# Performance work log

Hardware: AMD Instinct MI355X
Metric: run time of the kernel (lower is better)

## Reference

```python
import jax, jax.numpy as jnp
import numpy as np

# Faithful JAX port of the approxmatch EMD kernel (Fan et al.) wrapped by emdDist.
# 10 soft-assignment (auction-style) iterations with annealed temperature level=-4^j,
# j = 7..-1, final iteration level = 0. match is accumulated transport mass;
# cost[b] = sum_{k,l} match[b,k,l] * ||x1_k - x2_l||.

_EPS = 1e-9


def _approxmatch(xyz1, xyz2):
    # xyz1: (b, n, 3), xyz2: (b, m, 3)
    b, n, _ = xyz1.shape
    m = xyz2.shape[1]
    factorl = max(n, m) / n
    factorr = max(n, m) / m
    remainL = jnp.full((b, n), factorl, dtype=xyz1.dtype)   # mass left on xyz1 points
    remainR = jnp.full((b, m), factorr, dtype=xyz1.dtype)   # capacity left on xyz2 points
    # pairwise squared distances (b, n, m)
    d2 = jnp.sum((xyz1[:, :, None, :] - xyz2[:, None, :, :]) ** 2, axis=-1)
    match = jnp.zeros((b, n, m), dtype=xyz1.dtype)
    for j in range(7, -3, -1):  # j = 7, 6, ..., -1, -2
        level = 0.0 if j == -2 else -(4.0 ** j)
        # proposal weights from each left point, scaled by remaining right capacity
        w = jnp.exp(level * d2) * remainR[:, None, :]                      # (b,n,m)
        w = w / (jnp.sum(w, axis=-1, keepdims=True) + _EPS) * remainL[:, :, None]
        # right points accept at most their remaining capacity
        sumr = jnp.sum(w, axis=1) + _EPS                                   # (b,m)
        ratio = jnp.minimum(remainR / sumr, 1.0)                           # (b,m)
        delta = w * ratio[:, None, :]                                      # accepted transfer
        match = match + delta
        remainL = jnp.maximum(remainL - jnp.sum(delta, axis=-1), 0.0)
        remainR = jnp.maximum(remainR - jnp.sum(delta, axis=1), 0.0)
    return match, d2


def setup_inputs() -> dict:
    key = jax.random.key(0)
    k1, k2 = jax.random.split(key)
    B, N, M = 8, 4096, 4096
    input1 = jax.random.normal(k1, (B, N, 3), dtype=jnp.float32)
    input2 = jax.random.normal(k2, (B, M, 3), dtype=jnp.float32)
    return {"input1": input1, "input2": input2}


def reference(input1, input2):
    match, d2 = _approxmatch(input1, input2)
    # original CUDA backward treats match as a constant -> stop_gradient
    match = jax.lax.stop_gradient(match)
    dist = jnp.sqrt(jnp.maximum(d2, 1e-12))
    cost = jnp.sum(match * dist, axis=(1, 2))  # (b,)
    return cost
```

## Files before the change

### kernel.cpp

```cpp
#include <hip/hip_runtime.h>

#define NPTS 4096
#define NB   8
#define TPB  256
#define TPBR 128
#define MBLK 4
#define EPSC 1e-9f

#define EXP2(x)  __builtin_amdgcn_exp2f(x)
#define RCPF(x)  __builtin_amdgcn_rcpf(x)
#define SQRTF(x) __builtin_amdgcn_sqrtf(x)

__global__ __launch_bounds__(TPB) void sort_kernel(
    const float* __restrict__ x1, const float* __restrict__ x2,
    float4* __restrict__ x1p, float4* __restrict__ x2p)
{
  __shared__ unsigned int   hist[4096];
  __shared__ unsigned short codes[4096];
  __shared__ unsigned int   part[TPB];

  const int set = blockIdx.x, b = blockIdx.y;
  const float* src = set ? x2 : x1;
  float4* dst = set ? x2p : x1p;
  const int tid = threadIdx.x;

  for (int i = tid; i < 4096; i += TPB) hist[i] = 0;
  __syncthreads();

  for (int j = 0; j < NPTS / TPB; ++j) {
    int n = j * TPB + tid;
    const float* p = src + ((size_t)b * NPTS + n) * 3;
    float x = p[0], y = p[1], z = p[2];
    int qx = min(max((int)((x + 4.f) * 2.f), 0), 15);
    int qy = min(max((int)((y + 4.f) * 2.f), 0), 15);
    int qz = min(max((int)((z + 4.f) * 2.f), 0), 15);
    auto ex = [](int v) {
      return (v & 1) | ((v & 2) << 2) | ((v & 4) << 4) | ((v & 8) << 6);
    };
    int code = ex(qx) | (ex(qy) << 1) | (ex(qz) << 2);
    codes[n] = (unsigned short)code;
    atomicAdd(&hist[code], 1u);
  }
  __syncthreads();

  unsigned int loc[16], s = 0;
#pragma unroll
  for (int j = 0; j < 16; ++j) { loc[j] = s; s += hist[tid * 16 + j]; }
  part[tid] = s;
  __syncthreads();
  if (tid == 0) {
    unsigned int run = 0;
    for (int t = 0; t < TPB; ++t) { unsigned int v = part[t]; part[t] = run; run += v; }
  }
  __syncthreads();
  {
    unsigned int base = part[tid];
#pragma unroll
    for (int j = 0; j < 16; ++j) hist[tid * 16 + j] = base + loc[j];
  }
  __syncthreads();

  for (int j = 0; j < NPTS / TPB; ++j) {
    int n = j * TPB + tid;
    const float* p = src + ((size_t)b * NPTS + n) * 3;
    float x = p[0], y = p[1], z = p[2];
    unsigned int pos = atomicAdd(&hist[codes[n]], 1u);
    dst[(size_t)b * NPTS + pos] = make_float4(x, y, z, 0.f);
  }
}

template<int MODE, bool SKIP, int CHUNK>
__global__ __launch_bounds__(TPB) void ca_kernel(
    const float4* __restrict__ x2p, const float4* __restrict__ x1p,
    const float2* __restrict__ urP,
    float* __restrict__ dbufP, float* __restrict__ rsumP,
    float* __restrict__ out, float sc)
{
  __shared__ float4 x2s[CHUNK];
  __shared__ float2 urs[CHUNK];

  const int tid = threadIdx.x;
  const int nchunk = blockIdx.x, mseg = blockIdx.y, b = blockIdx.z;

  if (MODE == 0 && nchunk == 0 && mseg == 0 && tid == 0) out[b] = 0.f;

  for (int mm = tid; mm < CHUNK; mm += TPB) {
    int m = mseg * CHUNK + mm;
    float4 q = x2p[(size_t)b * NPTS + m];
    float sx = sc * q.x, sy = sc * q.y, sz = sc * q.z;
    float nq = fmaf(sz, sz, fmaf(sy, sy, sx * sx));
    x2s[mm] = make_float4(-2.f * sx, -2.f * sy, -2.f * sz, nq);
    urs[mm] = (MODE == 0) ? make_float2(0.f, 1.f) : urP[(size_t)b * NPTS + m];
  }
  __syncthreads();

  const int n0 = nchunk * (TPB * MBLK) + tid * MBLK;
  float px[MBLK], py[MBLK], pz[MBLK], np[MBLK], dacc[MBLK], racc[MBLK];
#pragma unroll
  for (int k = 0; k < MBLK; ++k) {
    float4 p = x1p[(size_t)b * NPTS + n0 + k];
    px[k] = sc * p.x; py[k] = sc * p.y; pz[k] = sc * p.z;
    np[k] = fmaf(pz[k], pz[k], fmaf(py[k], py[k], px[k] * px[k]));
    dacc[k] = 0.f; racc[k] = 0.f;
  }

#pragma unroll 4
  for (int mm = 0; mm < CHUNK; ++mm) {
    float4 q = x2s[mm];
    float2 ur = urs[mm];
    float ds2[MBLK];
#pragma unroll
    for (int k = 0; k < MBLK; ++k)
      ds2[k] = fmaf(q.x, px[k], fmaf(q.y, py[k], fmaf(q.z, pz[k], np[k] + q.w)));
    if (MODE == 2) {
#pragma unroll
      for (int k = 0; k < MBLK; ++k) {
        dacc[k] += ur.y;
        racc[k] = fmaf(EXP2(-ds2[k]), ur.x, racc[k]);
      }
    } else {
      bool go = true;
      if (SKIP) {
        float dmin = fminf(fminf(ds2[0], ds2[1]), fminf(ds2[2], ds2[3]));
        go = dmin < 126.f;
      }
      if (go) {
#pragma unroll
        for (int k = 0; k < MBLK; ++k) {
          float en = EXP2(-ds2[k]);
          dacc[k] = fmaf(en, ur.y, dacc[k]);
          if (MODE == 1) { float e2 = en * en; racc[k] = fmaf(e2 * e2, ur.x, racc[k]); }
        }
      }
    }
  }

  size_t base = ((size_t)mseg * NB + b) * NPTS + n0;
  *(float4*)&dbufP[base] = make_float4(dacc[0], dacc[1], dacc[2], dacc[3]);
  if (MODE >= 1)
    *(float4*)&rsumP[base] = make_float4(racc[0], racc[1], racc[2], racc[3]);
}

template<int LVL0, bool SKIP, int CHUNK>
__global__ __launch_bounds__(TPB) void b_kernel(
    const float4* __restrict__ x1p, const float* __restrict__ abuf,
    const float4* __restrict__ x2p,
    float* __restrict__ s0P, float* __restrict__ s1P,
    float sc, float inv_s)
{
  __shared__ float4 x1s[CHUNK];
  __shared__ float  as_[CHUNK];

  const int tid = threadIdx.x;
  const int mchunk = blockIdx.x, nsegi = blockIdx.y, b = blockIdx.z;

  for (int nn = tid; nn < CHUNK; nn += TPB) {
    int n = nsegi * CHUNK + nn;
    float4 p = x1p[(size_t)b * NPTS + n];
    float sx = sc * p.x, sy = sc * p.y, sz = sc * p.z;
    float npv = fmaf(sz, sz, fmaf(sy, sy, sx * sx));
    x1s[nn] = make_float4(-2.f * sx, -2.f * sy, -2.f * sz, npv);
    as_[nn] = abuf[(size_t)b * NPTS + n];
  }
  __syncthreads();

  const int m0 = mchunk * (TPB * MBLK) + tid * MBLK;
  float qx[MBLK], qy[MBLK], qz[MBLK], nq[MBLK], s0a[MBLK], s1a[MBLK];
#pragma unroll
  for (int k = 0; k < MBLK; ++k) {
    float4 q = x2p[(size_t)b * NPTS + m0 + k];
    qx[k] = sc * q.x; qy[k] = sc * q.y; qz[k] = sc * q.z;
    nq[k] = fmaf(qz[k], qz[k], fmaf(qy[k], qy[k], qx[k] * qx[k]));
    s0a[k] = 0.f; s1a[k] = 0.f;
  }

#pragma unroll 4
  for (int nn = 0; nn < CHUNK; ++nn) {
    float4 p = x1s[nn];
    float av = as_[nn];
    float ds2[MBLK];
#pragma unroll
    for (int k = 0; k < MBLK; ++k)
      ds2[k] = fmaf(p.x, qx[k], fmaf(p.y, qy[k], fmaf(p.z, qz[k], nq[k] + p.w)));
    if (LVL0) {
#pragma unroll
      for (int k = 0; k < MBLK; ++k) {
        s0a[k] += av;
        s1a[k] = fmaf(av, SQRTF(__builtin_fabsf(ds2[k])), s1a[k]);
      }
    } else {
      bool go = true;
      if (SKIP) {
        float dmin = fminf(fminf(ds2[0], ds2[1]), fminf(ds2[2], ds2[3]));
        go = dmin < 126.f;
      }
      if (go) {
#pragma unroll
        for (int k = 0; k < MBLK; ++k) {
          float tt = av * EXP2(-ds2[k]);
          s0a[k] += tt;
          s1a[k] = fmaf(tt, SQRTF(__builtin_fabsf(ds2[k])), s1a[k]);
        }
      }
    }
  }

  size_t base = ((size_t)nsegi * NB + b) * NPTS + m0;
  *(float4*)&s0P[base] = make_float4(s0a[0], s0a[1], s0a[2], s0a[3]);
  *(float4*)&s1P[base] = make_float4(s1a[0] * inv_s, s1a[1] * inv_s,
                                     s1a[2] * inv_s, s1a[3] * inv_s);
}

template<int NSEG>
__global__ __launch_bounds__(TPBR) void r1_kernel(
    const float* __restrict__ dbufP, const float* __restrict__ rsumP,
    float* __restrict__ lbuf, float* __restrict__ dtot,
    float* __restrict__ abuf, int iter)
{
  const int idx = blockIdx.x * TPBR + threadIdx.x;
  const int b = idx >> 12, n = idx & (NPTS - 1);
  const int off = b * NPTS + n;

  float dnew = 0.f;
#pragma unroll
  for (int s = 0; s < NSEG; ++s) dnew += dbufP[((size_t)s * NB + b) * NPTS + n];

  float rl;
  if (iter == 0) {
    rl = 1.f;
  } else {
    float rlp = lbuf[off];
    float ap  = rlp * RCPF(dtot[off] + EPSC);
    float rs = 0.f;
#pragma unroll
    for (int s = 0; s < NSEG; ++s) rs += rsumP[((size_t)s * NB + b) * NPTS + n];
    rl = fmaxf(rlp - ap * rs, 0.f);
  }
  lbuf[off] = rl;
  dtot[off] = dnew;
  abuf[off] = rl * RCPF(dnew + EPSC);
}

template<int NSEG, bool LAST>
__global__ __launch_bounds__(TPBR) void r2_kernel(
    const float* __restrict__ s0P, const float* __restrict__ s1P,
    float2* __restrict__ urbuf, float* __restrict__ out, int iter)
{
  __shared__ float red[TPBR];
  const int idx = blockIdx.x * TPBR + threadIdx.x;
  const int b = idx >> 12, m = idx & (NPTS - 1);
  const int off = b * NPTS + m;

  float s0 = 0.f, s1 = 0.f;
#pragma unroll
  for (int s = 0; s < NSEG; ++s) {
    s0 += s0P[((size_t)s * NB + b) * NPTS + m];
    s1 += s1P[((size_t)s * NB + b) * NPTS + m];
  }
  float rr    = (iter == 0) ? 1.f : urbuf[off].y;
  float sumr  = fmaf(rr, s0, EPSC);
  float ratio = fminf(rr * RCPF(sumr), 1.f);
  float u     = rr * ratio;
  if (!LAST) urbuf[off] = make_float2(u, fmaxf(rr - u * s0, 0.f));

  red[threadIdx.x] = u * s1;
  __syncthreads();
  for (int s = TPBR / 2; s > 0; s >>= 1) {
    if (threadIdx.x < s) red[threadIdx.x] += red[threadIdx.x + s];
    __syncthreads();
  }
  if (threadIdx.x == 0) atomicAdd(out + b, red[0]);
}

template<int NSEG>
static void run_all(const float* x1, const float* x2, float* out, float* ws,
                    hipStream_t stream)
{
  constexpr int CHUNK = NPTS / NSEG;
  const size_t plane = (size_t)NB * NPTS;

  float*  bufA = ws;
  float*  bufB = bufA + (size_t)NSEG * plane;
  float4* x1p  = (float4*)(bufB + (size_t)NSEG * plane);
  float4* x2p  = x1p + plane;
  float*  dtot = (float*)(x2p + plane);
  float*  lbuf = dtot + plane;
  float*  abuf = lbuf + plane;
  float2* urbuf = (float2*)(abuf + plane);

  const double L2E = 1.4426950408889634074;
  const double lv[10] = {-16384.0, -4096.0, -1024.0, -256.0, -64.0,
                         -16.0, -4.0, -1.0, -0.25, 0.0};
  float scl[10], inv_s[10];
  for (int i = 0; i < 10; ++i) {
    double c2 = lv[i] * L2E;
    scl[i]   = (i == 9) ? 1.f : (float)sqrt(-c2);
    inv_s[i] = (i == 9) ? 1.f : (float)(1.0 / sqrt(-c2));
  }

  dim3 gmain(NPTS / (TPB * MBLK), NSEG, NB), bmain(TPB);
  dim3 gr(NPTS * NB / TPBR), br(TPBR);

  sort_kernel<<<dim3(2, NB), bmain, 0, stream>>>(x1, x2, x1p, x2p);

  ca_kernel<0, true, CHUNK><<<gmain, bmain, 0, stream>>>(
      x2p, x1p, urbuf, bufA, bufB, out, scl[0]);

  for (int i = 0; i < 10; ++i) {
    r1_kernel<NSEG><<<gr, br, 0, stream>>>(bufA, bufB, lbuf, dtot, abuf, i);

    if (i <= 4)
      b_kernel<0, true, CHUNK><<<gmain, bmain, 0, stream>>>(
          x1p, abuf, x2p, bufA, bufB, scl[i], inv_s[i]);
    else if (i <= 8)
      b_kernel<0, false, CHUNK><<<gmain, bmain, 0, stream>>>(
          x1p, abuf, x2p, bufA, bufB, scl[i], inv_s[i]);
    else
      b_kernel<1, false, CHUNK><<<gmain, bmain, 0, stream>>>(
          x1p, abuf, x2p, bufA, bufB, 1.f, 1.f);

    if (i < 9)
      r2_kernel<NSEG, false><<<gr, br, 0, stream>>>(bufA, bufB, urbuf, out, i);
    else
      r2_kernel<NSEG, true><<<gr, br, 0, stream>>>(bufA, bufB, urbuf, out, i);

    if (i <= 3)
      ca_kernel<1, true, CHUNK><<<gmain, bmain, 0, stream>>>(
          x2p, x1p, urbuf, bufA, bufB, out, scl[i + 1]);
    else if (i <= 7)
      ca_kernel<1, false, CHUNK><<<gmain, bmain, 0, stream>>>(
          x2p, x1p, urbuf, bufA, bufB, out, scl[i + 1]);
    else if (i == 8)
      ca_kernel<2, false, CHUNK><<<gmain, bmain, 0, stream>>>(
          x2p, x1p, urbuf, bufA, bufB, out, scl[8]);
  }
}

extern "C" void kernel_launch(void* const* d_in, const int* in_sizes, int n_in,
                              void* d_out, int out_size, void* d_ws, size_t ws_size,
                              hipStream_t stream) {
  const float* x1 = (const float*)d_in[0];
  const float* x2 = (const float*)d_in[1];
  float* out = (float*)d_out;
  float* ws  = (float*)d_ws;

  const size_t plane = (size_t)NB * NPTS;
  auto need = [&](int nseg) {
    return (size_t)(2 * nseg + 13) * plane * sizeof(float);
  };

  if (ws_size >= need(64))      run_all<64>(x1, x2, out, ws, stream);
  else if (ws_size >= need(32)) run_all<32>(x1, x2, out, ws, stream);
  else                          run_all<16>(x1, x2, out, ws, stream);
}
```

Before: 989.8 us.

## Cull far tile pairs via bounding boxes and accumulate partials with atomics

Result: slower. 1.651 ms (+66.8%).

```diff
diff --git a/kernel.cpp b/kernel.cpp
--- a/kernel.cpp
+++ b/kernel.cpp
@@ -1,11 +1,13 @@
 #include <hip/hip_runtime.h>
 
-#define NPTS 4096
-#define NB   8
-#define TPB  256
-#define TPBR 128
-#define MBLK 4
-#define EPSC 1e-9f
+#define NPTS  4096
+#define NB    8
+#define TPB   256
+#define TPBR  256
+#define MBLK  4
+#define NSEG  64
+#define CHUNK 64
+#define EPSC  1e-9f
 
 #define EXP2(x)  __builtin_amdgcn_exp2f(x)
 #define RCPF(x)  __builtin_amdgcn_rcpf(x)
@@ -13,7 +15,10 @@
 
 __global__ __launch_bounds__(TPB) void sort_kernel(
     const float* __restrict__ x1, const float* __restrict__ x2,
-    float4* __restrict__ x1p, float4* __restrict__ x2p)
+    float4* __restrict__ x1p, float4* __restrict__ x2p,
+    float4* __restrict__ bb,
+    float* __restrict__ zacc,
+    float* __restrict__ out)
 {
   __shared__ unsigned int   hist[4096];
   __shared__ unsigned short codes[4096];
@@ -23,6 +28,11 @@
   const float* src = set ? x2 : x1;
   float4* dst = set ? x2p : x1p;
   const int tid = threadIdx.x;
+  const int bid = b * 2 + set;
+
+  for (int i = tid; i < 2 * NB * NPTS / 16; i += TPB)
+    zacc[(size_t)bid * (2 * NB * NPTS / 16) + i] = 0.f;
+  if (set == 0 && tid == 0) out[b] = 0.f;
 
   for (int i = tid; i < 4096; i += TPB) hist[i] = 0;
   __syncthreads();
@@ -30,10 +40,9 @@
   for (int j = 0; j < NPTS / TPB; ++j) {
     int n = j * TPB + tid;
     const float* p = src + ((size_t)b * NPTS + n) * 3;
-    float x = p[0], y = p[1], z = p[2];
-    int qx = min(max((int)((x + 4.f) * 2.f), 0), 15);
-    int qy = min(max((int)((y + 4.f) * 2.f), 0), 15);
-    int qz = min(max((int)((z + 4.f) * 2.f), 0), 15);
+    int qx = min(max((int)((p[0] + 4.f) * 2.f), 0), 15);
+    int qy = min(max((int)((p[1] + 4.f) * 2.f), 0), 15);
+    int qz = min(max((int)((p[2] + 4.f) * 2.f), 0), 15);
     auto ex = [](int v) {
       return (v & 1) | ((v & 2) << 2) | ((v & 4) << 4) | ((v & 8) << 6);
     };
@@ -63,26 +72,39 @@
   for (int j = 0; j < NPTS / TPB; ++j) {
     int n = j * TPB + tid;
     const float* p = src + ((size_t)b * NPTS + n) * 3;
-    float x = p[0], y = p[1], z = p[2];
     unsigned int pos = atomicAdd(&hist[codes[n]], 1u);
-    dst[(size_t)b * NPTS + pos] = make_float4(x, y, z, 0.f);
-  }
-}
-
-template<int MODE, bool SKIP, int CHUNK>
+    dst[(size_t)b * NPTS + pos] = make_float4(p[0], p[1], p[2], 0.f);
+  }
+  __syncthreads();
+
+  if (tid < 64) {
+    float mnx = 1e30f, mny = 1e30f, mnz = 1e30f;
+    float mxx = -1e30f, mxy = -1e30f, mxz = -1e30f;
+    for (int j = 0; j < CHUNK; ++j) {
+      float4 p = dst[(size_t)b * NPTS + tid * CHUNK + j];
+      mnx = fminf(mnx, p.x); mxx = fmaxf(mxx, p.x);
+      mny = fminf(mny, p.y); mxy = fmaxf(mxy, p.y);
+      mnz = fminf(mnz, p.z); mxz = fmaxf(mxz, p.z);
+    }
+    size_t bi = ((size_t)(set * NB + b) * 64 + tid) * 2;
+    bb[bi + 0] = make_float4(mnx, mny, mnz, 0.f);
+    bb[bi + 1] = make_float4(mxx, mxy, mxz, 0.f);
+  }
+}
+
+template<int MODE, bool CULL, bool PSKIP>
 __global__ __launch_bounds__(TPB) void ca_kernel(
     const float4* __restrict__ x2p, const float4* __restrict__ x1p,
-    const float2* __restrict__ urP,
-    float* __restrict__ dbufP, float* __restrict__ rsumP,
-    float* __restrict__ out, float sc)
+    const float2* __restrict__ urbuf,
+    float* __restrict__ dAcc, float* __restrict__ rAcc,
+    const float4* __restrict__ bb2,
+    float sc)
 {
   __shared__ float4 x2s[CHUNK];
   __shared__ float2 urs[CHUNK];
 
   const int tid = threadIdx.x;
   const int nchunk = blockIdx.x, mseg = blockIdx.y, b = blockIdx.z;
-
-  if (MODE == 0 && nchunk == 0 && mseg == 0 && tid == 0) out[b] = 0.f;
 
   for (int mm = tid; mm < CHUNK; mm += TPB) {
     int m = mseg * CHUNK + mm;
@@ -90,7 +112,8 @@
     float sx = sc * q.x, sy = sc * q.y, sz = sc * q.z;
     float nq = fmaf(sz, sz, fmaf(sy, sy, sx * sx));
     x2s[mm] = make_float4(-2.f * sx, -2.f * sy, -2.f * sz, nq);
-    urs[mm] = (MODE == 0) ? make_float2(0.f, 1.f) : urP[(size_t)b * NPTS + m];
+    urs[mm] = (MODE == 0) ? make_float2(0.f, 1.f)
+                          : urbuf[(size_t)b * NPTS + m];
   }
   __syncthreads();
 
@@ -104,6 +127,30 @@
     dacc[k] = 0.f; racc[k] = 0.f;
   }
 
+  if (CULL) {
+    float mnx = fminf(fminf(px[0], px[1]), fminf(px[2], px[3]));
+    float mny = fminf(fminf(py[0], py[1]), fminf(py[2], py[3]));
+    float mnz = fminf(fminf(pz[0], pz[1]), fminf(pz[2], pz[3]));
+    float mxx = fmaxf(fmaxf(px[0], px[1]), fmaxf(px[2], px[3]));
+    float mxy = fmaxf(fmaxf(py[0], py[1]), fmaxf(py[2], py[3]));
+    float mxz = fmaxf(fmaxf(pz[0], pz[1]), fmaxf(pz[2], pz[3]));
+#pragma unroll
+    for (int off = 1; off < 64; off <<= 1) {
+      mnx = fminf(mnx, __shfl_xor(mnx, off));
+      mny = fminf(mny, __shfl_xor(mny, off));
+      mnz = fminf(mnz, __shfl_xor(mnz, off));
+      mxx = fmaxf(mxx, __shfl_xor(mxx, off));
+      mxy = fmaxf(mxy, __shfl_xor(mxy, off));
+      mxz = fmaxf(mxz, __shfl_xor(mxz, off));
+    }
+    size_t bi = ((size_t)b * 64 + mseg) * 2;
+    float4 smin = bb2[bi + 0], smax = bb2[bi + 1];
+    float gx = fmaxf(0.f, fmaxf(sc * smin.x - mxx, mnx - sc * smax.x));
+    float gy = fmaxf(0.f, fmaxf(sc * smin.y - mxy, mny - sc * smax.y));
+    float gz = fmaxf(0.f, fmaxf(sc * smin.z - mxz, mnz - sc * smax.z));
+    if (fmaf(gx, gx, fmaf(gy, gy, gz * gz)) >= 126.f) return;
+  }
+
 #pragma unroll 4
   for (int mm = 0; mm < CHUNK; ++mm) {
     float4 q = x2s[mm];
@@ -120,7 +167,7 @@
       }
     } else {
       bool go = true;
-      if (SKIP) {
+      if (PSKIP) {
         float dmin = fminf(fminf(ds2[0], ds2[1]), fminf(ds2[2], ds2[3]));
         go = dmin < 126.f;
       }
@@ -135,17 +182,20 @@
     }
   }
 
-  size_t base = ((size_t)mseg * NB + b) * NPTS + n0;
-  *(float4*)&dbufP[base] = make_float4(dacc[0], dacc[1], dacc[2], dacc[3]);
-  if (MODE >= 1)
-    *(float4*)&rsumP[base] = make_float4(racc[0], racc[1], racc[2], racc[3]);
-}
-
-template<int LVL0, bool SKIP, int CHUNK>
+  size_t off = (size_t)b * NPTS + n0;
+#pragma unroll
+  for (int k = 0; k < MBLK; ++k) {
+    atomicAdd(&dAcc[off + k], dacc[k]);
+    if (MODE >= 1) atomicAdd(&rAcc[off + k], racc[k]);
+  }
+}
+
+template<int LVL0, bool CULL, bool PSKIP>
 __global__ __launch_bounds__(TPB) void b_kernel(
     const float4* __restrict__ x1p, const float* __restrict__ abuf,
     const float4* __restrict__ x2p,
-    float* __restrict__ s0P, float* __restrict__ s1P,
+    float* __restrict__ s0Acc, float* __restrict__ s1Acc,
+    const float4* __restrict__ bb1,
     float sc, float inv_s)
 {
   __shared__ float4 x1s[CHUNK];
@@ -174,6 +224,30 @@
     s0a[k] = 0.f; s1a[k] = 0.f;
   }
 
+  if (CULL) {
+    float mnx = fminf(fminf(qx[0], qx[1]), fminf(qx[2], qx[3]));
+    float mny = fminf(fminf(qy[0], qy[1]), fminf(qy[2], qy[3]));
+    float mnz = fminf(fminf(qz[0], qz[1]), fminf(qz[2], qz[3]));
+    float mxx = fmaxf(fmaxf(qx[0], qx[1]), fmaxf(qx[2], qx[3]));
+    float mxy = fmaxf(fmaxf(qy[0], qy[1]), fmaxf(qy[2], qy[3]));
+    float mxz = fmaxf(fmaxf(qz[0], qz[1]), fmaxf(qz[2], qz[3]));
+#pragma unroll
+    for (int off = 1; off < 64; off <<= 1) {
+      mnx = fminf(mnx, __shfl_xor(mnx, off));
+      mny = fminf(mny, __shfl_xor(mny, off));
+      mnz = fminf(mnz, __shfl_xor(mnz, off));
+      mxx = fmaxf(mxx, __shfl_xor(mxx, off));
+      mxy = fmaxf(mxy, __shfl_xor(mxy, off));
+      mxz = fmaxf(mxz, __shfl_xor(mxz, off));
+    }
+    size_t bi = ((size_t)b * 64 + nsegi) * 2;
+    float4 smin = bb1[bi + 0], smax = bb1[bi + 1];
+    float gx = fmaxf(0.f, fmaxf(sc * smin.x - mxx, mnx - sc * smax.x));
+    float gy = fmaxf(0.f, fmaxf(sc * smin.y - mxy, mny - sc * smax.y));
+    float gz = fmaxf(0.f, fmaxf(sc * smin.z - mxz, mnz - sc * smax.z));
+    if (fmaf(gx, gx, fmaf(gy, gy, gz * gz)) >= 126.f) return;
+  }
+
 #pragma unroll 4
   for (int nn = 0; nn < CHUNK; ++nn) {
     float4 p = x1s[nn];
@@ -190,7 +264,7 @@
       }
     } else {
       bool go = true;
-      if (SKIP) {
+      if (PSKIP) {
         float dmin = fminf(fminf(ds2[0], ds2[1]), fminf(ds2[2], ds2[3]));
         go = dmin < 126.f;
       }
@@ -205,63 +279,54 @@
     }
   }
 
-  size_t base = ((size_t)nsegi * NB + b) * NPTS + m0;
-  *(float4*)&s0P[base] = make_float4(s0a[0], s0a[1], s0a[2], s0a[3]);
-  *(float4*)&s1P[base] = make_float4(s1a[0] * inv_s, s1a[1] * inv_s,
-                                     s1a[2] * inv_s, s1a[3] * inv_s);
-}
-
-template<int NSEG>
+  size_t off = (size_t)b * NPTS + m0;
+#pragma unroll
+  for (int k = 0; k < MBLK; ++k) {
+    atomicAdd(&s0Acc[off + k], s0a[k]);
+    atomicAdd(&s1Acc[off + k], s1a[k] * inv_s);
+  }
+}
+
 __global__ __launch_bounds__(TPBR) void r1_kernel(
-    const float* __restrict__ dbufP, const float* __restrict__ rsumP,
+    const float* __restrict__ dAcc, const float* __restrict__ rAcc,
     float* __restrict__ lbuf, float* __restrict__ dtot,
-    float* __restrict__ abuf, int iter)
+    float* __restrict__ abuf,
+    float* __restrict__ s0Acc, float* __restrict__ s1Acc, int iter)
 {
   const int idx = blockIdx.x * TPBR + threadIdx.x;
-  const int b = idx >> 12, n = idx & (NPTS - 1);
-  const int off = b * NPTS + n;
-
-  float dnew = 0.f;
-#pragma unroll
-  for (int s = 0; s < NSEG; ++s) dnew += dbufP[((size_t)s * NB + b) * NPTS + n];
-
-  float rl;
-  if (iter == 0) {
-    rl = 1.f;
-  } else {
-    float rlp = lbuf[off];
-    float ap  = rlp * RCPF(dtot[off] + EPSC);
-    float rs = 0.f;
-#pragma unroll
-    for (int s = 0; s < NSEG; ++s) rs += rsumP[((size_t)s * NB + b) * NPTS + n];
-    rl = fmaxf(rlp - ap * rs, 0.f);
-  }
-  lbuf[off] = rl;
-  dtot[off] = dnew;
-  abuf[off] = rl * RCPF(dnew + EPSC);
-}
-
-template<int NSEG, bool LAST>
+  float dnew = dAcc[idx];
+  float rl = 1.f;
+  if (iter > 0) {
+    float rlp = lbuf[idx];
+    float ap  = rlp * RCPF(dtot[idx] + EPSC);
+    rl = fmaxf(rlp - ap * rAcc[idx], 0.f);
+  }
+  lbuf[idx] = rl;
+  dtot[idx] = dnew;
+  abuf[idx] = rl * RCPF(dnew + EPSC);
+  s0Acc[idx] = 0.f;
+  s1Acc[idx] = 0.f;
+}
+
+template<bool LAST>
 __global__ __launch_bounds__(TPBR) void r2_kernel(
-    const float* __restrict__ s0P, const float* __restrict__ s1P,
-    float2* __restrict__ urbuf, float* __restrict__ out, int iter)
+    const float* __restrict__ s0Acc, const float* __restrict__ s1Acc,
+    float2* __restrict__ urbuf,
+    float* __restrict__ dAcc, float* __restrict__ rAcc,
+    float* __restrict__ out, int iter)
 {
   __shared__ float red[TPBR];
   const int idx = blockIdx.x * TPBR + threadIdx.x;
-  const int b = idx >> 12, m = idx & (NPTS - 1);
-  const int off = b * NPTS + m;
-
-  float s0 = 0.f, s1 = 0.f;
-#pragma unroll
-  for (int s = 0; s < NSEG; ++s) {
-    s0 += s0P[((size_t)s * NB + b) * NPTS + m];
-    s1 += s1P[((size_t)s * NB + b) * NPTS + m];
-  }
-  float rr    = (iter == 0) ? 1.f : urbuf[off].y;
+  const int b = idx >> 12;
+
+  float s0 = s0Acc[idx], s1 = s1Acc[idx];
+  float rr    = (iter == 0) ? 1.f : urbuf[idx].y;
   float sumr  = fmaf(rr, s0, EPSC);
   float ratio = fminf(rr * RCPF(sumr), 1.f);
   float u     = rr * ratio;
-  if (!LAST) urbuf[off] = make_float2(u, fmaxf(rr - u * s0, 0.f));
+  if (!LAST) urbuf[idx] = make_float2(u, fmaxf(rr - u * s0, 0.f));
+  dAcc[idx] = 0.f;
+  rAcc[idx] = 0.f;
 
   red[threadIdx.x] = u * s1;
   __syncthreads();
@@ -272,21 +337,28 @@
   if (threadIdx.x == 0) atomicAdd(out + b, red[0]);
 }
 
-template<int NSEG>
-static void run_all(const float* x1, const float* x2, float* out, float* ws,
-                    hipStream_t stream)
-{
-  constexpr int CHUNK = NPTS / NSEG;
+extern "C" void kernel_launch(void* const* d_in, const int* in_sizes, int n_in,
+                              void* d_out, int out_size, void* d_ws, size_t ws_size,
+                              hipStream_t stream) {
+  const float* x1 = (const float*)d_in[0];
+  const float* x2 = (const float*)d_in[1];
+  float* out = (float*)d_out;
+
   const size_t plane = (size_t)NB * NPTS;
-
-  float*  bufA = ws;
-  float*  bufB = bufA + (size_t)NSEG * plane;
-  float4* x1p  = (float4*)(bufB + (size_t)NSEG * plane);
-  float4* x2p  = x1p + plane;
-  float*  dtot = (float*)(x2p + plane);
-  float*  lbuf = dtot + plane;
-  float*  abuf = lbuf + plane;
+  float*  ws    = (float*)d_ws;
+  float*  dAcc  = ws;
+  float*  rAcc  = dAcc + plane;
+  float*  s0Acc = rAcc + plane;
+  float*  s1Acc = s0Acc + plane;
+  float*  dtot  = s1Acc + plane;
+  float*  lbuf  = dtot + plane;
+  float*  abuf  = lbuf + plane;
   float2* urbuf = (float2*)(abuf + plane);
+  float4* x1p   = (float4*)(urbuf + plane);
+  float4* x2p   = x1p + plane;
+  float4* bb    = x2p + plane;
+  float4* bb1   = bb;
+  float4* bb2   = bb + (size_t)NB * 64 * 2;
 
   const double L2E = 1.4426950408889634074;
   const double lv[10] = {-16384.0, -4096.0, -1024.0, -256.0, -64.0,
@@ -299,57 +371,48 @@
   }
 
   dim3 gmain(NPTS / (TPB * MBLK), NSEG, NB), bmain(TPB);
-  dim3 gr(NPTS * NB / TPBR), br(TPBR);
-
-  sort_kernel<<<dim3(2, NB), bmain, 0, stream>>>(x1, x2, x1p, x2p);
-
-  ca_kernel<0, true, CHUNK><<<gmain, bmain, 0, stream>>>(
-      x2p, x1p, urbuf, bufA, bufB, out, scl[0]);
+  dim3 gr(NB * NPTS / TPBR), br(TPBR);
+
+  sort_kernel<<<dim3(2, NB), bmain, 0, stream>>>(x1, x2, x1p, x2p, bb, dAcc, out);
+
+  ca_kernel<0, true, true><<<gmain, bmain, 0, stream>>>(
+      x2p, x1p, urbuf, dAcc, rAcc, bb2, scl[0]);
 
   for (int i = 0; i < 10; ++i) {
-    r1_kernel<NSEG><<<gr, br, 0, stream>>>(bufA, bufB, lbuf, dtot, abuf, i);
+    r1_kernel<<<gr, br, 0, stream>>>(dAcc, rAcc, lbuf, dtot, abuf,
+                                     s0Acc, s1Acc, i);
 
     if (i <= 4)
-      b_kernel<0, true, CHUNK><<<gmain, bmain, 0, stream>>>(
-          x1p, abuf, x2p, bufA, bufB, scl[i], inv_s[i]);
+      b_kernel<0, true, true><<<gmain, bmain, 0, stream>>>(
+          x1p, abuf, x2p, s0Acc, s1Acc, bb1, scl[i], inv_s[i]);
+    else if (i == 5)
+      b_kernel<0, true, false><<<gmain, bmain, 0, stream>>>(
+          x1p, abuf, x2p, s0Acc, s1Acc, bb1, scl[i], inv_s[i]);
     else if (i <= 8)
-      b_kernel<0, false, CHUNK><<<gmain, bmain, 0, stream>>>(
-          x1p, abuf, x2p, bufA, bufB, scl[i], inv_s[i]);
+      b_kernel<0, false, false><<<gmain, bmain, 0, stream>>>(
+          x1p, abuf, x2p, s0Acc, s1Acc, bb1, scl[i], inv_s[i]);
     else
-      b_kernel<1, false, CHUNK><<<gmain, bmain, 0, stream>>>(
-          x1p, abuf, x2p, bufA, bufB, 1.f, 1.f);
+      b_kernel<1, false, false><<<gmain, bmain, 0, stream>>>(
+          x1p, abuf, x2p, s0Acc, s1Acc, bb1, 1.f, 1.f);
 
     if (i < 9)
-      r2_kernel<NSEG, false><<<gr, br, 0, stream>>>(bufA, bufB, urbuf, out, i);
+      r2_kernel<false><<<gr, br, 0, stream>>>(s0Acc, s1Acc, urbuf,
+                                              dAcc, rAcc, out, i);
     else
-      r2_kernel<NSEG, true><<<gr, br, 0, stream>>>(bufA, bufB, urbuf, out, i);
+      r2_kernel<true><<<gr, br, 0, stream>>>(s0Acc, s1Acc, urbuf,
+                                             dAcc, rAcc, out, i);
 
     if (i <= 3)
-      ca_kernel<1, true, CHUNK><<<gmain, bmain, 0, stream>>>(
-          x2p, x1p, urbuf, bufA, bufB, out, scl[i + 1]);
+      ca_kernel<1, true, true><<<gmain, bmain, 0, stream>>>(
+          x2p, x1p, urbuf, dAcc, rAcc, bb2, scl[i + 1]);
+    else if (i == 4)
+      ca_kernel<1, true, false><<<gmain, bmain, 0, stream>>>(
+          x2p, x1p, urbuf, dAcc, rAcc, bb2, scl[i + 1]);
     else if (i <= 7)
-      ca_kernel<1, false, CHUNK><<<gmain, bmain, 0, stream>>>(
-          x2p, x1p, urbuf, bufA, bufB, out, scl[i + 1]);
+      ca_kernel<1, false, false><<<gmain, bmain, 0, stream>>>(
+          x2p, x1p, urbuf, dAcc, rAcc, bb2, scl[i + 1]);
     else if (i == 8)
-      ca_kernel<2, false, CHUNK><<<gmain, bmain, 0, stream>>>(
-          x2p, x1p, urbuf, bufA, bufB, out, scl[8]);
-  }
-}
-
-extern "C" void kernel_launch(void* const* d_in, const int* in_sizes, int n_in,
-                              void* d_out, int out_size, void* d_ws, size_t ws_size,
-                              hipStream_t stream) {
-  const float* x1 = (const float*)d_in[0];
-  const float* x2 = (const float*)d_in[1];
-  float* out = (float*)d_out;
-  float* ws  = (float*)d_ws;
-
-  const size_t plane = (size_t)NB * NPTS;
-  auto need = [&](int nseg) {
-    return (size_t)(2 * nseg + 13) * plane * sizeof(float);
-  };
-
-  if (ws_size >= need(64))      run_all<64>(x1, x2, out, ws, stream);
-  else if (ws_size >= need(32)) run_all<32>(x1, x2, out, ws, stream);
-  else                          run_all<16>(x1, x2, out, ws, stream);
-}
+      ca_kernel<2, false, false><<<gmain, bmain, 0, stream>>>(
+          x2p, x1p, urbuf, dAcc, rAcc, bb2, scl[8]);
+  }
+}
```

## Cull whole waves against per-segment bounding boxes of sorted points

Applied to the files above, without the earlier changes.

Result: slower. 1.010 ms (+2.0%).

```diff
diff --git a/kernel.cpp b/kernel.cpp
--- a/kernel.cpp
+++ b/kernel.cpp
@@ -13,7 +13,8 @@
 
 __global__ __launch_bounds__(TPB) void sort_kernel(
     const float* __restrict__ x1, const float* __restrict__ x2,
-    float4* __restrict__ x1p, float4* __restrict__ x2p)
+    float4* __restrict__ x1p, float4* __restrict__ x2p,
+    float4* __restrict__ bb)
 {
   __shared__ unsigned int   hist[4096];
   __shared__ unsigned short codes[4096];
@@ -30,10 +31,9 @@
   for (int j = 0; j < NPTS / TPB; ++j) {
     int n = j * TPB + tid;
     const float* p = src + ((size_t)b * NPTS + n) * 3;
-    float x = p[0], y = p[1], z = p[2];
-    int qx = min(max((int)((x + 4.f) * 2.f), 0), 15);
-    int qy = min(max((int)((y + 4.f) * 2.f), 0), 15);
-    int qz = min(max((int)((z + 4.f) * 2.f), 0), 15);
+    int qx = min(max((int)((p[0] + 4.f) * 2.f), 0), 15);
+    int qy = min(max((int)((p[1] + 4.f) * 2.f), 0), 15);
+    int qz = min(max((int)((p[2] + 4.f) * 2.f), 0), 15);
     auto ex = [](int v) {
       return (v & 1) | ((v & 2) << 2) | ((v & 4) << 4) | ((v & 8) << 6);
     };
@@ -63,18 +63,58 @@
   for (int j = 0; j < NPTS / TPB; ++j) {
     int n = j * TPB + tid;
     const float* p = src + ((size_t)b * NPTS + n) * 3;
-    float x = p[0], y = p[1], z = p[2];
     unsigned int pos = atomicAdd(&hist[codes[n]], 1u);
-    dst[(size_t)b * NPTS + pos] = make_float4(x, y, z, 0.f);
-  }
-}
-
-template<int MODE, bool SKIP, int CHUNK>
+    dst[(size_t)b * NPTS + pos] = make_float4(p[0], p[1], p[2], 0.f);
+  }
+  __syncthreads();
+
+  if (tid < 64) {
+    float mnx = 1e30f, mny = 1e30f, mnz = 1e30f;
+    float mxx = -1e30f, mxy = -1e30f, mxz = -1e30f;
+    for (int j = 0; j < 64; ++j) {
+      float4 p = dst[(size_t)b * NPTS + tid * 64 + j];
+      mnx = fminf(mnx, p.x); mxx = fmaxf(mxx, p.x);
+      mny = fminf(mny, p.y); mxy = fmaxf(mxy, p.y);
+      mnz = fminf(mnz, p.z); mxz = fmaxf(mxz, p.z);
+    }
+    size_t bi = ((size_t)(set * NB + b) * 64 + tid) * 2;
+    bb[bi + 0] = make_float4(mnx, mny, mnz, 0.f);
+    bb[bi + 1] = make_float4(mxx, mxy, mxz, 0.f);
+  }
+}
+
+__device__ __forceinline__ bool wave_cull(
+    const float px[MBLK], const float py[MBLK], const float pz[MBLK],
+    const float4* bbg, size_t gi, float sc)
+{
+  float mnx = fminf(fminf(px[0], px[1]), fminf(px[2], px[3]));
+  float mny = fminf(fminf(py[0], py[1]), fminf(py[2], py[3]));
+  float mnz = fminf(fminf(pz[0], pz[1]), fminf(pz[2], pz[3]));
+  float mxx = fmaxf(fmaxf(px[0], px[1]), fmaxf(px[2], px[3]));
+  float mxy = fmaxf(fmaxf(py[0], py[1]), fmaxf(py[2], py[3]));
+  float mxz = fmaxf(fmaxf(pz[0], pz[1]), fmaxf(pz[2], pz[3]));
+#pragma unroll
+  for (int off = 1; off < 64; off <<= 1) {
+    mnx = fminf(mnx, __shfl_xor(mnx, off));
+    mny = fminf(mny, __shfl_xor(mny, off));
+    mnz = fminf(mnz, __shfl_xor(mnz, off));
+    mxx = fmaxf(mxx, __shfl_xor(mxx, off));
+    mxy = fmaxf(mxy, __shfl_xor(mxy, off));
+    mxz = fmaxf(mxz, __shfl_xor(mxz, off));
+  }
+  float4 smin = bbg[gi * 2 + 0], smax = bbg[gi * 2 + 1];
+  float gx = fmaxf(0.f, fmaxf(sc * smin.x - mxx, mnx - sc * smax.x));
+  float gy = fmaxf(0.f, fmaxf(sc * smin.y - mxy, mny - sc * smax.y));
+  float gz = fmaxf(0.f, fmaxf(sc * smin.z - mxz, mnz - sc * smax.z));
+  return fmaf(gx, gx, fmaf(gy, gy, gz * gz)) >= 126.f;
+}
+
+template<int MODE, bool CULL, bool PSKIP, int CHUNK>
 __global__ __launch_bounds__(TPB) void ca_kernel(
     const float4* __restrict__ x2p, const float4* __restrict__ x1p,
-    const float2* __restrict__ urP,
+    const float2* __restrict__ urbuf,
     float* __restrict__ dbufP, float* __restrict__ rsumP,
-    float* __restrict__ out, float sc)
+    const float4* __restrict__ bb2, float* __restrict__ out, float sc)
 {
   __shared__ float4 x2s[CHUNK];
   __shared__ float2 urs[CHUNK];
@@ -90,7 +130,7 @@
     float sx = sc * q.x, sy = sc * q.y, sz = sc * q.z;
     float nq = fmaf(sz, sz, fmaf(sy, sy, sx * sx));
     x2s[mm] = make_float4(-2.f * sx, -2.f * sy, -2.f * sz, nq);
-    urs[mm] = (MODE == 0) ? make_float2(0.f, 1.f) : urP[(size_t)b * NPTS + m];
+    urs[mm] = (MODE == 0) ? make_float2(0.f, 1.f) : urbuf[(size_t)b * NPTS + m];
   }
   __syncthreads();
 
@@ -104,6 +144,15 @@
     dacc[k] = 0.f; racc[k] = 0.f;
   }
 
+  size_t base = ((size_t)mseg * NB + b) * NPTS + n0;
+  if (CULL) {
+    if (wave_cull(px, py, pz, bb2 + (size_t)b * 128, mseg, sc)) {
+      *(float4*)&dbufP[base] = make_float4(0.f, 0.f, 0.f, 0.f);
+      if (MODE >= 1) *(float4*)&rsumP[base] = make_float4(0.f, 0.f, 0.f, 0.f);
+      return;
+    }
+  }
+
 #pragma unroll 4
   for (int mm = 0; mm < CHUNK; ++mm) {
     float4 q = x2s[mm];
@@ -120,7 +169,7 @@
       }
     } else {
       bool go = true;
-      if (SKIP) {
+      if (PSKIP) {
         float dmin = fminf(fminf(ds2[0], ds2[1]), fminf(ds2[2], ds2[3]));
         go = dmin < 126.f;
       }
@@ -135,18 +184,17 @@
     }
   }
 
-  size_t base = ((size_t)mseg * NB + b) * NPTS + n0;
   *(float4*)&dbufP[base] = make_float4(dacc[0], dacc[1], dacc[2], dacc[3]);
   if (MODE >= 1)
     *(float4*)&rsumP[base] = make_float4(racc[0], racc[1], racc[2], racc[3]);
 }
 
-template<int LVL0, bool SKIP, int CHUNK>
+template<int LVL0, bool CULL, bool PSKIP, int CHUNK>
 __global__ __launch_bounds__(TPB) void b_kernel(
     const float4* __restrict__ x1p, const float* __restrict__ abuf,
     const float4* __restrict__ x2p,
     float* __restrict__ s0P, float* __restrict__ s1P,
-    float sc, float inv_s)
+    const float4* __restrict__ bb1, float sc, float inv_s)
 {
   __shared__ float4 x1s[CHUNK];
   __shared__ float  as_[CHUNK];
@@ -174,6 +222,15 @@
     s0a[k] = 0.f; s1a[k] = 0.f;
   }
 
+  size_t base = ((size_t)nsegi * NB + b) * NPTS + m0;
+  if (CULL) {
+    if (wave_cull(qx, qy, qz, bb1 + (size_t)b * 128, nsegi, sc)) {
+      *(float4*)&s0P[base] = make_float4(0.f, 0.f, 0.f, 0.f);
+      *(float4*)&s1P[base] = make_float4(0.f, 0.f, 0.f, 0.f);
+      return;
+    }
+  }
+
 #pragma unroll 4
   for (int nn = 0; nn < CHUNK; ++nn) {
     float4 p = x1s[nn];
@@ -190,7 +247,7 @@
       }
     } else {
       bool go = true;
-      if (SKIP) {
+      if (PSKIP) {
         float dmin = fminf(fminf(ds2[0], ds2[1]), fminf(ds2[2], ds2[3]));
         go = dmin < 126.f;
       }
@@ -205,7 +262,6 @@
     }
   }
 
-  size_t base = ((size_t)nsegi * NB + b) * NPTS + m0;
   *(float4*)&s0P[base] = make_float4(s0a[0], s0a[1], s0a[2], s0a[3]);
   *(float4*)&s1P[base] = make_float4(s1a[0] * inv_s, s1a[1] * inv_s,
                                      s1a[2] * inv_s, s1a[3] * inv_s);
@@ -287,6 +343,9 @@
   float*  lbuf = dtot + plane;
   float*  abuf = lbuf + plane;
   float2* urbuf = (float2*)(abuf + plane);
+  float4* bb   = (float4*)(urbuf + plane);
+  float4* bb1  = bb;
+  float4* bb2  = bb + (size_t)NB * 128;
 
   const double L2E = 1.4426950408889634074;
   const double lv[10] = {-16384.0, -4096.0, -1024.0, -256.0, -64.0,
@@ -301,23 +360,26 @@
   dim3 gmain(NPTS / (TPB * MBLK), NSEG, NB), bmain(TPB);
   dim3 gr(NPTS * NB / TPBR), br(TPBR);
 
-  sort_kernel<<<dim3(2, NB), bmain, 0, stream>>>(x1, x2, x1p, x2p);
-
-  ca_kernel<0, true, CHUNK><<<gmain, bmain, 0, stream>>>(
-      x2p, x1p, urbuf, bufA, bufB, out, scl[0]);
+  sort_kernel<<<dim3(2, NB), bmain, 0, stream>>>(x1, x2, x1p, x2p, bb);
+
+  ca_kernel<0, true, true, CHUNK><<<gmain, bmain, 0, stream>>>(
+      x2p, x1p, urbuf, bufA, bufB, bb2, out, scl[0]);
 
   for (int i = 0; i < 10; ++i) {
     r1_kernel<NSEG><<<gr, br, 0, stream>>>(bufA, bufB, lbuf, dtot, abuf, i);
 
     if (i <= 4)
-      b_kernel<0, true, CHUNK><<<gmain, bmain, 0, stream>>>(
-          x1p, abuf, x2p, bufA, bufB, scl[i], inv_s[i]);
+      b_kernel<0, true, true, CHUNK><<<gmain, bmain, 0, stream>>>(
+          x1p, abuf, x2p, bufA, bufB, bb1, scl[i], inv_s[i]);
+    else if (i == 5)
+      b_kernel<0, true, false, CHUNK><<<gmain, bmain, 0, stream>>>(
+          x1p, abuf, x2p, bufA, bufB, bb1, scl[i], inv_s[i]);
     else if (i <= 8)
-      b_kernel<0, false, CHUNK><<<gmain, bmain, 0, stream>>>(
-          x1p, abuf, x2p, bufA, bufB, scl[i], inv_s[i]);
+      b_kernel<0, false, false, CHUNK><<<gmain, bmain, 0, stream>>>(
+          x1p, abuf, x2p, bufA, bufB, bb1, scl[i], inv_s[i]);
     else
-      b_kernel<1, false, CHUNK><<<gmain, bmain, 0, stream>>>(
-          x1p, abuf, x2p, bufA, bufB, 1.f, 1.f);
+      b_kernel<1, false, false, CHUNK><<<gmain, bmain, 0, stream>>>(
+          x1p, abuf, x2p, bufA, bufB, bb1, 1.f, 1.f);
 
     if (i < 9)
       r2_kernel<NSEG, false><<<gr, br, 0, stream>>>(bufA, bufB, urbuf, out, i);
@@ -325,14 +387,17 @@
       r2_kernel<NSEG, true><<<gr, br, 0, stream>>>(bufA, bufB, urbuf, out, i);
 
     if (i <= 3)
-      ca_kernel<1, true, CHUNK><<<gmain, bmain, 0, stream>>>(
-          x2p, x1p, urbuf, bufA, bufB, out, scl[i + 1]);
+      ca_kernel<1, true, true, CHUNK><<<gmain, bmain, 0, stream>>>(
+          x2p, x1p, urbuf, bufA, bufB, bb2, out, scl[i + 1]);
+    else if (i <= 5)
+      ca_kernel<1, true, false, CHUNK><<<gmain, bmain, 0, stream>>>(
+          x2p, x1p, urbuf, bufA, bufB, bb2, out, scl[i + 1]);
     else if (i <= 7)
-      ca_kernel<1, false, CHUNK><<<gmain, bmain, 0, stream>>>(
-          x2p, x1p, urbuf, bufA, bufB, out, scl[i + 1]);
+      ca_kernel<1, false, false, CHUNK><<<gmain, bmain, 0, stream>>>(
+          x2p, x1p, urbuf, bufA, bufB, bb2, out, scl[i + 1]);
     else if (i == 8)
-      ca_kernel<2, false, CHUNK><<<gmain, bmain, 0, stream>>>(
-          x2p, x1p, urbuf, bufA, bufB, out, scl[8]);
+      ca_kernel<2, false, false, CHUNK><<<gmain, bmain, 0, stream>>>(
+          x2p, x1p, urbuf, bufA, bufB, bb2, out, scl[8]);
   }
 }
 
@@ -346,7 +411,8 @@
 
   const size_t plane = (size_t)NB * NPTS;
   auto need = [&](int nseg) {
-    return (size_t)(2 * nseg + 13) * plane * sizeof(float);
+    return (size_t)(2 * nseg + 13) * plane * sizeof(float)
+         + (size_t)2048 * sizeof(float4);
   };
 
   if (ws_size >= need(64))      run_all<64>(x1, x2, out, ws, stream);
```
